# Optimization experiments

Measured on AMD Instinct MI355X. Metric: run time of the kernel, lower is better.

The kernel has to match this reference:

```python
import jax, jax.numpy as jnp
import numpy as np

TOP_K = 2


def setup_inputs() -> dict:
    key = jax.random.key(0)
    ks = jax.random.split(key, 5)
    T, H, I, E = 4096, 2048, 4096, 8
    scale = 0.02
    return {
        "hidden_states": jax.random.normal(ks[0], (T, H), dtype=jnp.float32),
        "router_logits": jax.random.normal(ks[1], (T, E), dtype=jnp.float32),
        "w1": jax.random.normal(ks[2], (E, I, H), dtype=jnp.float32) * scale,
        "w3": jax.random.normal(ks[3], (E, I, H), dtype=jnp.float32) * scale,
        "w2": jax.random.normal(ks[4], (E, H, I), dtype=jnp.float32) * scale,
    }


def reference(hidden_states, router_logits, w1, w3, w2):
    # hidden_states: [T, H], router_logits: [T, E]
    E = w1.shape[0]
    # Top-k routing with softmax renormalization over the selected logits.
    topk_vals, topk_idx = jax.lax.top_k(router_logits, TOP_K)  # [T, K]
    routing_weights = jax.nn.softmax(topk_vals, axis=-1)       # [T, K]
    # combine[t, e] = sum of routing weights of slots that picked expert e
    combine = jnp.sum(
        jnp.where(topk_idx[:, :, None] == jnp.arange(E)[None, None, :],
                  routing_weights[:, :, None], 0.0),
        axis=1)  # [T, E]
    out = jnp.zeros_like(hidden_states)
    for e in range(E):  # fixed small structural loop over experts
        gate = hidden_states @ w1[e].T        # [T, I]
        up = hidden_states @ w3[e].T          # [T, I]
        y = (jax.nn.silu(gate) * up) @ w2[e].T  # [T, H]
        out = out + combine[:, e, None] * y
    return out
```

## Files before the change

### kernel.cpp

```cpp
#include <hip/hip_runtime.h>
#include <stdint.h>

#define T_TOK 4096
#define H_DIM 2048
#define I_DIM 4096
#define N_EXP 8

typedef __attribute__((ext_vector_type(8))) short bf16x8;
typedef __attribute__((ext_vector_type(4))) float f32x4;
typedef __attribute__((ext_vector_type(8))) unsigned short u16x8;

__device__ __forceinline__ unsigned short f2bf(float x) {
    union { float f; unsigned u; } v; v.f = x;
    unsigned r = v.u + 0x7FFF + ((v.u >> 16) & 1);
    return (unsigned short)(r >> 16);
}

__device__ __forceinline__ u16x8 cvt8(float4 a, float4 b) {
    u16x8 o;
    o[0] = f2bf(a.x); o[1] = f2bf(a.y); o[2] = f2bf(a.z); o[3] = f2bf(a.w);
    o[4] = f2bf(b.x); o[5] = f2bf(b.y); o[6] = f2bf(b.z); o[7] = f2bf(b.w);
    return o;
}

__device__ __forceinline__ void async_cp16(const void* g, const unsigned short* lds_base) {
    __builtin_amdgcn_global_load_lds(
        (const __attribute__((address_space(1))) unsigned*)g,
        (__attribute__((address_space(3))) unsigned*)(unsigned)(uintptr_t)lds_base,
        16, 0, 0);
}

__global__ void routing_kernel(const float* __restrict__ logits,
                               int* __restrict__ counts, int* __restrict__ offsets,
                               int* __restrict__ btok, float* __restrict__ bw,
                               int* __restrict__ tok2slot) {
    __shared__ int s_cnt[N_EXP];
    __shared__ int s_off[N_EXP];
    __shared__ int s_cur[N_EXP];
    const int tid = threadIdx.x;
    if (tid < N_EXP) s_cnt[tid] = 0;
    __syncthreads();

    int e0a[16], e1a[16]; float w0a[16], w1a[16];
    #pragma unroll
    for (int it = 0; it < 16; ++it) {
        int t = tid + it * 256;
        float l[8];
        #pragma unroll
        for (int e = 0; e < 8; ++e) l[e] = logits[t * 8 + e];
        int b0 = 0; float v0 = l[0];
        #pragma unroll
        for (int e = 1; e < 8; ++e) if (l[e] > v0) { v0 = l[e]; b0 = e; }
        int b1 = (b0 == 0) ? 1 : 0; float v1 = l[b1];
        #pragma unroll
        for (int e = 0; e < 8; ++e) if (e != b0 && l[e] > v1) { v1 = l[e]; b1 = e; }
        float w0 = 1.0f / (1.0f + __expf(v1 - v0));
        e0a[it] = b0; e1a[it] = b1; w0a[it] = w0; w1a[it] = 1.0f - w0;
        atomicAdd(&s_cnt[b0], 1);
        atomicAdd(&s_cnt[b1], 1);
    }
    __syncthreads();
    if (tid == 0) {
        int acc = 0;
        for (int e = 0; e < N_EXP; ++e) { s_off[e] = acc; s_cur[e] = acc; acc += s_cnt[e]; }
    }
    __syncthreads();
    if (tid < N_EXP) { counts[tid] = s_cnt[tid]; offsets[tid] = s_off[tid]; }
    #pragma unroll
    for (int it = 0; it < 16; ++it) {
        int t = tid + it * 256;
        int p0 = atomicAdd(&s_cur[e0a[it]], 1);
        btok[p0] = t; bw[p0] = w0a[it];
        int p1 = atomicAdd(&s_cur[e1a[it]], 1);
        btok[p1] = t; bw[p1] = w1a[it];
        tok2slot[2 * t] = p0;
        tok2slot[2 * t + 1] = p1;
    }
}

__global__ void cvt_kernel(const float* __restrict__ x, unsigned short* __restrict__ xb) {
    int i = blockIdx.x * blockDim.x + threadIdx.x;
    float4 a = ((const float4*)x)[2 * i];
    float4 b = ((const float4*)x)[2 * i + 1];
    ((u16x8*)xb)[i] = cvt8(a, b);
}


__global__ __launch_bounds__(256, 2)
void gemm1p_kernel(const unsigned short* __restrict__ Xb,
                   const float* __restrict__ W1,
                   const float* __restrict__ W3,
                   const int* __restrict__ counts,
                   const int* __restrict__ offsets,
                   const int* __restrict__ btok,
                   unsigned short* __restrict__ hbuf) {
    const int e = blockIdx.z;
    const int ne = counts[e];
    const int mt = blockIdx.y;
    if (mt * 128 >= ne) return;
    const int nt = blockIdx.x;
    const int off = offsets[e];

    __shared__ unsigned short sA[3][128 * 32];
    __shared__ unsigned short sB1[3][128 * 32];
    __shared__ unsigned short sB3[3][128 * 32];

    const int tid = threadIdx.x;
    const int lane = tid & 63;
    const int wv = tid >> 6;
    const int wm = (wv >> 1) << 6;
    const int wn = (wv & 1) << 6;
    const int q = lane >> 4;
    const int c = lane & 15;
    const int xq = q ^ ((c >> 1) & 3);

    const int aoff = (wm + c) * 32 + xq * 8;
    const int boff = (wn + c) * 32 + xq * 8;

    const int arow = wv * 16 + (lane >> 2);
    const int sgA = (lane & 3) ^ ((lane >> 3) & 3);

    int sl0 = mt * 128 + arow;       if (sl0 >= ne) sl0 = ne - 1;
    int sl1 = mt * 128 + arow + 64;  if (sl1 >= ne) sl1 = ne - 1;
    const unsigned short* gA0 = Xb + (size_t)btok[off + sl0] * H_DIM + sgA * 8;
    const unsigned short* gA1 = Xb + (size_t)btok[off + sl1] * H_DIM + sgA * 8;
    const int dofsA0 = wv * 512;
    const int dofsA1 = 2048 + wv * 512;

    const int brow = tid >> 2;
    const int sgB = (tid & 3) ^ ((tid >> 3) & 3);
    const size_t wrow = (size_t)e * I_DIM + nt * 128 + brow;
    const float* gW1  = W1 + wrow * H_DIM + (tid & 3) * 8;
    const float* gW1b = gW1 + (size_t)64 * H_DIM;
    const float* gW3  = W3 + wrow * H_DIM + (tid & 3) * 8;
    const float* gW3b = gW3 + (size_t)64 * H_DIM;
    const int bwro  = brow * 32 + sgB * 8;
    const int bwro2 = bwro + 2048;

    f32x4 accg[4][4], accu[4][4];
    const f32x4 zero = {0.0f, 0.0f, 0.0f, 0.0f};
    #pragma unroll
    for (int i = 0; i < 4; ++i)
        #pragma unroll
        for (int j = 0; j < 4; ++j) { accg[i][j] = zero; accu[i][j] = zero; }

    float4 w0, w1, w2, w3, w4, w5, w6, w7;

    #pragma unroll
    for (int h = 0; h < 2; ++h) {
        const float* p1  = gW1  + h * 32;
        const float* p1b = gW1b + h * 32;
        const float* p3  = gW3  + h * 32;
        const float* p3b = gW3b + h * 32;
        *(u16x8*)(&sB1[h][bwro])  = cvt8(((const float4*)p1)[0],  ((const float4*)p1)[1]);
        *(u16x8*)(&sB1[h][bwro2]) = cvt8(((const float4*)p1b)[0], ((const float4*)p1b)[1]);
        *(u16x8*)(&sB3[h][bwro])  = cvt8(((const float4*)p3)[0],  ((const float4*)p3)[1]);
        *(u16x8*)(&sB3[h][bwro2]) = cvt8(((const float4*)p3b)[0], ((const float4*)p3b)[1]);
    }
    async_cp16(gA0,      &sA[0][dofsA0]);
    async_cp16(gA1,      &sA[0][dofsA1]);
    async_cp16(gA0 + 32, &sA[1][dofsA0]);
    async_cp16(gA1 + 32, &sA[1][dofsA1]);
    w0 = ((const float4*)(gW1  + 64))[0]; w1 = ((const float4*)(gW1  + 64))[1];
    w2 = ((const float4*)(gW1b + 64))[0]; w3 = ((const float4*)(gW1b + 64))[1];
    w4 = ((const float4*)(gW3  + 64))[0]; w5 = ((const float4*)(gW3  + 64))[1];
    w6 = ((const float4*)(gW3b + 64))[0]; w7 = ((const float4*)(gW3b + 64))[1];

    asm volatile("s_waitcnt lgkmcnt(0)" ::: "memory");
    asm volatile("s_waitcnt vmcnt(10)" ::: "memory");
    __builtin_amdgcn_s_barrier();
    __builtin_amdgcn_sched_barrier(0);

    const int NT = H_DIM / 32;

#define G1_PH(H, S, S2)                                                                              \
    {                                                                                                \
        if ((H) + 2 < NT) {                                                                          \
            *(u16x8*)(&sB1[S2][bwro])  = cvt8(w0, w1);                                               \
            *(u16x8*)(&sB1[S2][bwro2]) = cvt8(w2, w3);                                               \
            *(u16x8*)(&sB3[S2][bwro])  = cvt8(w4, w5);                                               \
            *(u16x8*)(&sB3[S2][bwro2]) = cvt8(w6, w7);                                               \
        }                                                                                            \
        if ((H) + 3 < NT) {                                                                          \
            const float* p1  = gW1  + (size_t)((H) + 3) * 32;                                        \
            const float* p1b = gW1b + (size_t)((H) + 3) * 32;                                        \
            const float* p3  = gW3  + (size_t)((H) + 3) * 32;                                        \
            const float* p3b = gW3b + (size_t)((H) + 3) * 32;                                        \
            w0 = ((const float4*)p1)[0];  w1 = ((const float4*)p1)[1];                               \
            w2 = ((const float4*)p1b)[0]; w3 = ((const float4*)p1b)[1];                              \
            w4 = ((const float4*)p3)[0];  w5 = ((const float4*)p3)[1];                               \
            w6 = ((const float4*)p3b)[0]; w7 = ((const float4*)p3b)[1];                              \
        }                                                                                            \
        bf16x8 af[4], b1f[4], b3f[4];                                                                \
        _Pragma("unroll")                                                                            \
        for (int i = 0; i < 4; ++i) af[i]  = *(const bf16x8*)(&sA[S][aoff + i * 512]);               \
        _Pragma("unroll")                                                                            \
        for (int j = 0; j < 4; ++j) b1f[j] = *(const bf16x8*)(&sB1[S][boff + j * 512]);              \
        _Pragma("unroll")                                                                            \
        for (int j = 0; j < 4; ++j) b3f[j] = *(const bf16x8*)(&sB3[S][boff + j * 512]);              \
        if ((H) + 2 < NT) {                                                                          \
            async_cp16(gA0 + ((H) + 2) * 32, &sA[S2][dofsA0]);                                       \
            async_cp16(gA1 + ((H) + 2) * 32, &sA[S2][dofsA1]);                                       \
        }                                                                                            \
        __builtin_amdgcn_sched_barrier(0);                                                           \
        __builtin_amdgcn_s_setprio(1);                                                               \
        _Pragma("unroll")                                                                            \
        for (int i = 0; i < 4; ++i)                                                                  \
            _Pragma("unroll")                                                                        \
            for (int j = 0; j < 4; ++j)                                                              \
                accg[i][j] = __builtin_amdgcn_mfma_f32_16x16x32_bf16(af[i], b1f[j], accg[i][j], 0, 0, 0); \
        _Pragma("unroll")                                                                            \
        for (int i = 0; i < 4; ++i)                                                                  \
            _Pragma("unroll")                                                                        \
            for (int j = 0; j < 4; ++j)                                                              \
                accu[i][j] = __builtin_amdgcn_mfma_f32_16x16x32_bf16(af[i], b3f[j], accu[i][j], 0, 0, 0); \
        __builtin_amdgcn_s_setprio(0);                                                               \
        if ((H) + 1 < NT) {                                                                          \
            asm volatile("s_waitcnt lgkmcnt(0)" ::: "memory");                                       \
            if ((H) + 3 < NT)      asm volatile("s_waitcnt vmcnt(10)" ::: "memory");                 \
            else if ((H) + 2 < NT) asm volatile("s_waitcnt vmcnt(2)" ::: "memory");                  \
            else                   asm volatile("s_waitcnt vmcnt(0)" ::: "memory");                  \
            __builtin_amdgcn_s_barrier();                                                            \
            __builtin_amdgcn_sched_barrier(0);                                                       \
        }                                                                                            \
    }

    int h = 0;
    for (int t = 0; t < 21; ++t) {
        G1_PH(h,     0, 2);
        G1_PH(h + 1, 1, 0);
        G1_PH(h + 2, 2, 1);
        h += 3;
    }
    G1_PH(63, 0, 2);
#undef G1_PH

    #pragma unroll
    for (int i = 0; i < 4; ++i) {
        #pragma unroll
        for (int r = 0; r < 4; ++r) {
            int mloc = wm + i * 16 + q * 4 + r;
            int slot = mt * 128 + mloc;
            if (slot < ne) {
                size_t rowbase = (size_t)(off + slot) * I_DIM + nt * 128 + wn;
                #pragma unroll
                for (int j = 0; j < 4; ++j) {
                    float g = accg[i][j][r];
                    float u = accu[i][j][r];
                    float val = (g / (1.0f + __expf(-g))) * u;
                    hbuf[rowbase + j * 16 + c] = f2bf(val);
                }
            }
        }
    }
}

__global__ __launch_bounds__(256, 3)
void gemm2p_kernel(const unsigned short* __restrict__ hbuf,
                   const float* __restrict__ W2,
                   const int* __restrict__ counts,
                   const int* __restrict__ offsets,
                   const int* __restrict__ btok,
                   const float* __restrict__ bw,
                   float* __restrict__ out) {
    const int e = blockIdx.z;
    const int ne = counts[e];
    const int mt = blockIdx.y;
    if (mt * 128 >= ne) return;
    const int nt = blockIdx.x;
    const int off = offsets[e];

    __shared__ unsigned short sA[3][128 * 32];
    __shared__ unsigned short sB[3][128 * 32];

    const int tid = threadIdx.x;
    const int lane = tid & 63;
    const int wv = tid >> 6;
    const int wm = (wv >> 1) << 6;
    const int wn = (wv & 1) << 6;
    const int q = lane >> 4;
    const int c = lane & 15;
    const int xq = q ^ ((c >> 1) & 3);

    const int aoff = (wm + c) * 32 + xq * 8;
    const int boff = (wn + c) * 32 + xq * 8;

    const int arow = wv * 16 + (lane >> 2);
    const int sgA = (lane & 3) ^ ((lane >> 3) & 3);
    int sl0 = mt * 128 + arow;       if (sl0 >= ne) sl0 = ne - 1;
    int sl1 = mt * 128 + arow + 64;  if (sl1 >= ne) sl1 = ne - 1;
    const unsigned short* gA0 = hbuf + (size_t)(off + sl0) * I_DIM + sgA * 8;
    const unsigned short* gA1 = hbuf + (size_t)(off + sl1) * I_DIM + sgA * 8;
    const int dofsA0 = wv * 512;
    const int dofsA1 = 2048 + wv * 512;

    const int brow = tid >> 2;
    const int sgB = (tid & 3) ^ ((tid >> 3) & 3);
    const size_t wrow = (size_t)e * H_DIM + nt * 128 + brow;
    const float* gB  = W2 + wrow * I_DIM + (tid & 3) * 8;
    const float* gBb = gB + (size_t)64 * I_DIM;
    const int bwro  = brow * 32 + sgB * 8;
    const int bwro2 = bwro + 2048;

    f32x4 acc[4][4];
    const f32x4 zero = {0.0f, 0.0f, 0.0f, 0.0f};
    #pragma unroll
    for (int i = 0; i < 4; ++i)
        #pragma unroll
        for (int j = 0; j < 4; ++j) acc[i][j] = zero;

    float4 w0, w1, w2, w3;

    #pragma unroll
    for (int h = 0; h < 2; ++h) {
        const float* p  = gB  + h * 32;
        const float* pb = gBb + h * 32;
        *(u16x8*)(&sB[h][bwro])  = cvt8(((const float4*)p)[0],  ((const float4*)p)[1]);
        *(u16x8*)(&sB[h][bwro2]) = cvt8(((const float4*)pb)[0], ((const float4*)pb)[1]);
    }
    async_cp16(gA0,      &sA[0][dofsA0]);
    async_cp16(gA1,      &sA[0][dofsA1]);
    async_cp16(gA0 + 32, &sA[1][dofsA0]);
    async_cp16(gA1 + 32, &sA[1][dofsA1]);
    w0 = ((const float4*)(gB  + 64))[0]; w1 = ((const float4*)(gB  + 64))[1];
    w2 = ((const float4*)(gBb + 64))[0]; w3 = ((const float4*)(gBb + 64))[1];

    asm volatile("s_waitcnt lgkmcnt(0)" ::: "memory");
    asm volatile("s_waitcnt vmcnt(6)" ::: "memory");
    __builtin_amdgcn_s_barrier();
    __builtin_amdgcn_sched_barrier(0);

    const int NT = I_DIM / 32;

#define G2_PH(H, S, S2)                                                                              \
    {                                                                                                \
        if ((H) + 2 < NT) {                                                                          \
            *(u16x8*)(&sB[S2][bwro])  = cvt8(w0, w1);                                                \
            *(u16x8*)(&sB[S2][bwro2]) = cvt8(w2, w3);                                                \
        }                                                                                            \
        if ((H) + 3 < NT) {                                                                          \
            const float* p  = gB  + (size_t)((H) + 3) * 32;                                          \
            const float* pb = gBb + (size_t)((H) + 3) * 32;                                          \
            w0 = ((const float4*)p)[0];  w1 = ((const float4*)p)[1];                                 \
            w2 = ((const float4*)pb)[0]; w3 = ((const float4*)pb)[1];                                \
        }                                                                                            \
        bf16x8 af[4], bfr[4];                                                                        \
        _Pragma("unroll")                                                                            \
        for (int i = 0; i < 4; ++i) af[i]  = *(const bf16x8*)(&sA[S][aoff + i * 512]);               \
        _Pragma("unroll")                                                                            \
        for (int j = 0; j < 4; ++j) bfr[j] = *(const bf16x8*)(&sB[S][boff + j * 512]);               \
        if ((H) + 2 < NT) {                                                                          \
            async_cp16(gA0 + ((H) + 2) * 32, &sA[S2][dofsA0]);                                       \
            async_cp16(gA1 + ((H) + 2) * 32, &sA[S2][dofsA1]);                                       \
        }                                                                                            \
        __builtin_amdgcn_sched_barrier(0);                                                           \
        __builtin_amdgcn_s_setprio(1);                                                               \
        _Pragma("unroll")                                                                            \
        for (int i = 0; i < 4; ++i)                                                                  \
            _Pragma("unroll")                                                                        \
            for (int j = 0; j < 4; ++j)                                                              \
                acc[i][j] = __builtin_amdgcn_mfma_f32_16x16x32_bf16(af[i], bfr[j], acc[i][j], 0, 0, 0); \
        __builtin_amdgcn_s_setprio(0);                                                               \
        if ((H) + 1 < NT) {                                                                          \
            asm volatile("s_waitcnt lgkmcnt(0)" ::: "memory");                                       \
            if ((H) + 3 < NT)      asm volatile("s_waitcnt vmcnt(6)" ::: "memory");                  \
            else if ((H) + 2 < NT) asm volatile("s_waitcnt vmcnt(2)" ::: "memory");                  \
            else                   asm volatile("s_waitcnt vmcnt(0)" ::: "memory");                  \
            __builtin_amdgcn_s_barrier();                                                            \
            __builtin_amdgcn_sched_barrier(0);                                                       \
        }                                                                                            \
    }

    int h = 0;
    for (int t = 0; t < 42; ++t) {
        G2_PH(h,     0, 2);
        G2_PH(h + 1, 1, 0);
        G2_PH(h + 2, 2, 1);
        h += 3;
    }
    G2_PH(126, 0, 2);
    G2_PH(127, 1, 0);
#undef G2_PH

    #pragma unroll
    for (int i = 0; i < 4; ++i) {
        #pragma unroll
        for (int r = 0; r < 4; ++r) {
            int mloc = wm + i * 16 + q * 4 + r;
            int slot = mt * 128 + mloc;
            if (slot < ne) {
                int tok = btok[off + slot];
                float wgt = bw[off + slot];
                float* obase = out + (size_t)tok * H_DIM + nt * 128 + wn;
                #pragma unroll
                for (int j = 0; j < 4; ++j)
                    atomicAdd(obase + j * 16 + c, wgt * acc[i][j][r]);
            }
        }
    }
}


__global__ __launch_bounds__(256, 2)
void gemm1_kernel(const unsigned short* __restrict__ Xb,
                  const float* __restrict__ W1,
                  const float* __restrict__ W3,
                  const int* __restrict__ counts,
                  const int* __restrict__ offsets,
                  const int* __restrict__ btok,
                  unsigned short* __restrict__ hbuf) {
    const int e = blockIdx.z;
    const int ne = counts[e];
    const int mt = blockIdx.y;
    if (mt * 128 >= ne) return;
    const int nt = blockIdx.x;
    const int off = offsets[e];

    __shared__ unsigned short sA[128][32];
    __shared__ unsigned short sB1[128][32];
    __shared__ unsigned short sB3[128][32];
    __shared__ int s_tok[128];

    const int tid = threadIdx.x;
    if (tid < 128) {
        int slot = mt * 128 + tid;
        s_tok[tid] = (slot < ne) ? btok[off + slot] : -1;
    }

    const float* __restrict__ pB1 = W1 + (size_t)e * I_DIM * H_DIM + (size_t)(nt * 128) * H_DIM;
    const float* __restrict__ pB3 = W3 + (size_t)e * I_DIM * H_DIM + (size_t)(nt * 128) * H_DIM;

    const int lane = tid & 63;
    const int wv = tid >> 6;
    const int wm = (wv >> 1) << 6;
    const int wn = (wv & 1) << 6;
    const int q = lane >> 4;
    const int c = lane & 15;

    f32x4 accg[4][4], accu[4][4];
    const f32x4 zero = {0.0f, 0.0f, 0.0f, 0.0f};
    #pragma unroll
    for (int i = 0; i < 4; ++i)
        #pragma unroll
        for (int j = 0; j < 4; ++j) { accg[i][j] = zero; accu[i][j] = zero; }

    const int srow = tid >> 2;
    const int schunk = (tid & 3) * 8;

    for (int kt = 0; kt < H_DIM; kt += 32) {
        __syncthreads();
        #pragma unroll
        for (int p = 0; p < 2; ++p) {
            int r = srow + p * 64;
            int tok = s_tok[r];
            u16x8 av = {0, 0, 0, 0, 0, 0, 0, 0};
            if (tok >= 0)
                av = *(const u16x8*)(Xb + (size_t)tok * H_DIM + kt + schunk);
            *(u16x8*)(&sA[r][schunk]) = av;

            const float* b1 = pB1 + (size_t)r * H_DIM + kt + schunk;
            *(u16x8*)(&sB1[r][schunk]) = cvt8(*(const float4*)(b1), *(const float4*)(b1 + 4));

            const float* b3 = pB3 + (size_t)r * H_DIM + kt + schunk;
            *(u16x8*)(&sB3[r][schunk]) = cvt8(*(const float4*)(b3), *(const float4*)(b3 + 4));
        }
        __syncthreads();

        bf16x8 af[4], b1f[4], b3f[4];
        #pragma unroll
        for (int i = 0; i < 4; ++i)
            af[i] = *(const bf16x8*)(&sA[wm + i * 16 + c][q * 8]);
        #pragma unroll
        for (int j = 0; j < 4; ++j) {
            b1f[j] = *(const bf16x8*)(&sB1[wn + j * 16 + c][q * 8]);
            b3f[j] = *(const bf16x8*)(&sB3[wn + j * 16 + c][q * 8]);
        }
        #pragma unroll
        for (int i = 0; i < 4; ++i)
            #pragma unroll
            for (int j = 0; j < 4; ++j) {
                accg[i][j] = __builtin_amdgcn_mfma_f32_16x16x32_bf16(af[i], b1f[j], accg[i][j], 0, 0, 0);
                accu[i][j] = __builtin_amdgcn_mfma_f32_16x16x32_bf16(af[i], b3f[j], accu[i][j], 0, 0, 0);
            }
    }

    #pragma unroll
    for (int i = 0; i < 4; ++i) {
        #pragma unroll
        for (int r = 0; r < 4; ++r) {
            int mloc = wm + i * 16 + q * 4 + r;
            int slot = mt * 128 + mloc;
            if (slot < ne) {
                size_t rowbase = (size_t)(off + slot) * I_DIM + nt * 128 + wn;
                #pragma unroll
                for (int j = 0; j < 4; ++j) {
                    float g = accg[i][j][r];
                    float u = accu[i][j][r];
                    float val = (g / (1.0f + __expf(-g))) * u;
                    hbuf[rowbase + j * 16 + c] = f2bf(val);
                }
            }
        }
    }
}

__global__ __launch_bounds__(256, 2)
void gemm2_kernel(const unsigned short* __restrict__ hbuf,
                  const float* __restrict__ W2,
                  const int* __restrict__ counts,
                  const int* __restrict__ offsets,
                  const int* __restrict__ btok,
                  const float* __restrict__ bw,
                  float* __restrict__ out) {
    const int e = blockIdx.z;
    const int ne = counts[e];
    const int mt = blockIdx.y;
    if (mt * 128 >= ne) return;
    const int nt = blockIdx.x;
    const int off = offsets[e];

    __shared__ unsigned short sA[128][32];
    __shared__ unsigned short sB[128][32];

    const int tid = threadIdx.x;
    const int lane = tid & 63;
    const int wv = tid >> 6;
    const int wm = (wv >> 1) << 6;
    const int wn = (wv & 1) << 6;
    const int q = lane >> 4;
    const int c = lane & 15;

    const float* __restrict__ pB = W2 + (size_t)e * H_DIM * I_DIM + (size_t)(nt * 128) * I_DIM;

    f32x4 acc[4][4];
    const f32x4 zero = {0.0f, 0.0f, 0.0f, 0.0f};
    #pragma unroll
    for (int i = 0; i < 4; ++i)
        #pragma unroll
        for (int j = 0; j < 4; ++j) acc[i][j] = zero;

    const int srow = tid >> 2;
    const int schunk = (tid & 3) * 8;

    for (int kt = 0; kt < I_DIM; kt += 32) {
        __syncthreads();
        #pragma unroll
        for (int p = 0; p < 2; ++p) {
            int r = srow + p * 64;
            int slot = mt * 128 + r;
            u16x8 av = {0, 0, 0, 0, 0, 0, 0, 0};
            if (slot < ne)
                av = *(const u16x8*)(hbuf + (size_t)(off + slot) * I_DIM + kt + schunk);
            *(u16x8*)(&sA[r][schunk]) = av;

            const float* b = pB + (size_t)r * I_DIM + kt + schunk;
            *(u16x8*)(&sB[r][schunk]) = cvt8(*(const float4*)(b), *(const float4*)(b + 4));
        }
        __syncthreads();

        bf16x8 af[4], bfr[4];
        #pragma unroll
        for (int i = 0; i < 4; ++i)
            af[i] = *(const bf16x8*)(&sA[wm + i * 16 + c][q * 8]);
        #pragma unroll
        for (int j = 0; j < 4; ++j)
            bfr[j] = *(const bf16x8*)(&sB[wn + j * 16 + c][q * 8]);
        #pragma unroll
        for (int i = 0; i < 4; ++i)
            #pragma unroll
            for (int j = 0; j < 4; ++j)
                acc[i][j] = __builtin_amdgcn_mfma_f32_16x16x32_bf16(af[i], bfr[j], acc[i][j], 0, 0, 0);
    }

    #pragma unroll
    for (int i = 0; i < 4; ++i) {
        #pragma unroll
        for (int r = 0; r < 4; ++r) {
            int mloc = wm + i * 16 + q * 4 + r;
            int slot = mt * 128 + mloc;
            if (slot < ne) {
                int tok = btok[off + slot];
                float wgt = bw[off + slot];
                float* obase = out + (size_t)tok * H_DIM + nt * 128 + wn;
                #pragma unroll
                for (int j = 0; j < 4; ++j)
                    atomicAdd(obase + j * 16 + c, wgt * acc[i][j][r]);
            }
        }
    }
}


extern "C" void kernel_launch(void* const* d_in, const int* in_sizes, int n_in,
                              void* d_out, int out_size, void* d_ws, size_t ws_size,
                              hipStream_t stream) {
    const float* hs = (const float*)d_in[0];
    const float* rl = (const float*)d_in[1];
    const float* w1 = (const float*)d_in[2];
    const float* w3 = (const float*)d_in[3];
    const float* w2 = (const float*)d_in[4];
    float* out = (float*)d_out;

    char* ws = (char*)d_ws;
    int*   counts   = (int*)(ws);
    int*   offsets  = (int*)(ws + 256);
    int*   btok     = (int*)(ws + 4096);
    float* bw       = (float*)(ws + 36864);
    int*   tok2slot = (int*)(ws + 69632);

    const size_t MB = 1ull << 20;
    const size_t NEED_A = 146 * MB;

    if (ws_size >= NEED_A) {
        unsigned short* Xb   = (unsigned short*)(ws + 1 * MB);
        unsigned short* hbuf = (unsigned short*)(ws + 17 * MB);

        hipMemsetAsync(out, 0, (size_t)T_TOK * H_DIM * sizeof(float), stream);

        routing_kernel<<<1, 256, 0, stream>>>(rl, counts, offsets, btok, bw, tok2slot);

        cvt_kernel<<<(T_TOK * H_DIM / 8) / 256, 256, 0, stream>>>(hs, Xb);

        gemm1p_kernel<<<dim3(I_DIM / 128, 64, N_EXP), 256, 0, stream>>>(
            Xb, w1, w3, counts, offsets, btok, hbuf);

        gemm2p_kernel<<<dim3(H_DIM / 128, 64, N_EXP), 256, 0, stream>>>(
            hbuf, w2, counts, offsets, btok, bw, out);
    } else {
        unsigned short* Xb   = (unsigned short*)(ws + 1 * MB);
        unsigned short* hbuf = (unsigned short*)(ws + 32 * MB);

        hipMemsetAsync(out, 0, (size_t)T_TOK * H_DIM * sizeof(float), stream);

        routing_kernel<<<1, 256, 0, stream>>>(rl, counts, offsets, btok, bw, tok2slot);

        cvt_kernel<<<(T_TOK * H_DIM / 8) / 256, 256, 0, stream>>>(hs, Xb);

        gemm1_kernel<<<dim3(I_DIM / 128, T_TOK / 128, N_EXP), 256, 0, stream>>>(
            Xb, w1, w3, counts, offsets, btok, hbuf);

        gemm2_kernel<<<dim3(H_DIM / 128, T_TOK / 128, N_EXP), 256, 0, stream>>>(
            hbuf, w2, counts, offsets, btok, bw, out);
    }
}
```

Measured before the change: 1.245 ms.

## Widen gemm2p output tile to 256 columns for more A-tile reuse

Doubles the N tile of the down-projection GEMM from 128 to 256 columns. Each warp now computes a 64x128 sub-tile with twice as many MFMA accumulators, and each block loads and converts four W2 row groups per K step. The aim is to reuse each loaded hbuf A tile across twice as many output columns, halving A traffic and the block count. In exchange it raises register and LDS use (occupancy bound drops from 3 to 2) and halves the number of blocks in the grid.

```diff
diff --git a/kernel.cpp b/kernel.cpp
--- a/kernel.cpp
+++ b/kernel.cpp
@@ -255,7 +255,7 @@
     }
 }
 
-__global__ __launch_bounds__(256, 3)
+__global__ __launch_bounds__(256, 2)
 void gemm2p_kernel(const unsigned short* __restrict__ hbuf,
                    const float* __restrict__ W2,
                    const int* __restrict__ counts,
@@ -271,13 +271,13 @@
     const int off = offsets[e];
 
     __shared__ unsigned short sA[3][128 * 32];
-    __shared__ unsigned short sB[3][128 * 32];
+    __shared__ unsigned short sB[3][256 * 32];
 
     const int tid = threadIdx.x;
     const int lane = tid & 63;
     const int wv = tid >> 6;
     const int wm = (wv >> 1) << 6;
-    const int wn = (wv & 1) << 6;
+    const int wn = (wv & 1) << 7;
     const int q = lane >> 4;
     const int c = lane & 15;
     const int xq = q ^ ((c >> 1) & 3);
@@ -296,37 +296,44 @@
 
     const int brow = tid >> 2;
     const int sgB = (tid & 3) ^ ((tid >> 3) & 3);
-    const size_t wrow = (size_t)e * H_DIM + nt * 128 + brow;
-    const float* gB  = W2 + wrow * I_DIM + (tid & 3) * 8;
-    const float* gBb = gB + (size_t)64 * I_DIM;
+    const size_t wrow = (size_t)e * H_DIM + nt * 256 + brow;
+    const float* gB0 = W2 + wrow * I_DIM + (tid & 3) * 8;
+    const float* gB1 = gB0 + (size_t)64  * I_DIM;
+    const float* gB2 = gB0 + (size_t)128 * I_DIM;
+    const float* gB3 = gB0 + (size_t)192 * I_DIM;
     const int bwro  = brow * 32 + sgB * 8;
-    const int bwro2 = bwro + 2048;
-
-    f32x4 acc[4][4];
+
+    f32x4 acc[4][8];
     const f32x4 zero = {0.0f, 0.0f, 0.0f, 0.0f};
     #pragma unroll
     for (int i = 0; i < 4; ++i)
         #pragma unroll
-        for (int j = 0; j < 4; ++j) acc[i][j] = zero;
-
-    float4 w0, w1, w2, w3;
+        for (int j = 0; j < 8; ++j) acc[i][j] = zero;
+
+    float4 w0, w1, w2, w3, w4, w5, w6, w7;
 
     #pragma unroll
     for (int h = 0; h < 2; ++h) {
-        const float* p  = gB  + h * 32;
-        const float* pb = gBb + h * 32;
-        *(u16x8*)(&sB[h][bwro])  = cvt8(((const float4*)p)[0],  ((const float4*)p)[1]);
-        *(u16x8*)(&sB[h][bwro2]) = cvt8(((const float4*)pb)[0], ((const float4*)pb)[1]);
+        const float* p0 = gB0 + h * 32;
+        const float* p1 = gB1 + h * 32;
+        const float* p2 = gB2 + h * 32;
+        const float* p3 = gB3 + h * 32;
+        *(u16x8*)(&sB[h][bwro])        = cvt8(((const float4*)p0)[0], ((const float4*)p0)[1]);
+        *(u16x8*)(&sB[h][bwro + 2048]) = cvt8(((const float4*)p1)[0], ((const float4*)p1)[1]);
+        *(u16x8*)(&sB[h][bwro + 4096]) = cvt8(((const float4*)p2)[0], ((const float4*)p2)[1]);
+        *(u16x8*)(&sB[h][bwro + 6144]) = cvt8(((const float4*)p3)[0], ((const float4*)p3)[1]);
     }
     async_cp16(gA0,      &sA[0][dofsA0]);
     async_cp16(gA1,      &sA[0][dofsA1]);
     async_cp16(gA0 + 32, &sA[1][dofsA0]);
     async_cp16(gA1 + 32, &sA[1][dofsA1]);
-    w0 = ((const float4*)(gB  + 64))[0]; w1 = ((const float4*)(gB  + 64))[1];
-    w2 = ((const float4*)(gBb + 64))[0]; w3 = ((const float4*)(gBb + 64))[1];
+    w0 = ((const float4*)(gB0 + 64))[0]; w1 = ((const float4*)(gB0 + 64))[1];
+    w2 = ((const float4*)(gB1 + 64))[0]; w3 = ((const float4*)(gB1 + 64))[1];
+    w4 = ((const float4*)(gB2 + 64))[0]; w5 = ((const float4*)(gB2 + 64))[1];
+    w6 = ((const float4*)(gB3 + 64))[0]; w7 = ((const float4*)(gB3 + 64))[1];
 
     asm volatile("s_waitcnt lgkmcnt(0)" ::: "memory");
-    asm volatile("s_waitcnt vmcnt(6)" ::: "memory");
+    asm volatile("s_waitcnt vmcnt(10)" ::: "memory");
     __builtin_amdgcn_s_barrier();
     __builtin_amdgcn_sched_barrier(0);
 
@@ -335,20 +342,26 @@
 #define G2_PH(H, S, S2)                                                                              \
     {                                                                                                \
         if ((H) + 2 < NT) {                                                                          \
-            *(u16x8*)(&sB[S2][bwro])  = cvt8(w0, w1);                                                \
-            *(u16x8*)(&sB[S2][bwro2]) = cvt8(w2, w3);                                                \
+            *(u16x8*)(&sB[S2][bwro])        = cvt8(w0, w1);                                          \
+            *(u16x8*)(&sB[S2][bwro + 2048]) = cvt8(w2, w3);                                          \
+            *(u16x8*)(&sB[S2][bwro + 4096]) = cvt8(w4, w5);                                          \
+            *(u16x8*)(&sB[S2][bwro + 6144]) = cvt8(w6, w7);                                          \
         }                                                                                            \
         if ((H) + 3 < NT) {                                                                          \
-            const float* p  = gB  + (size_t)((H) + 3) * 32;                                          \
-            const float* pb = gBb + (size_t)((H) + 3) * 32;                                          \
-            w0 = ((const float4*)p)[0];  w1 = ((const float4*)p)[1];                                 \
-            w2 = ((const float4*)pb)[0]; w3 = ((const float4*)pb)[1];                                \
-        }                                                                                            \
-        bf16x8 af[4], bfr[4];                                                                        \
+            const float* p0 = gB0 + (size_t)((H) + 3) * 32;                                          \
+            const float* p1 = gB1 + (size_t)((H) + 3) * 32;                                          \
+            const float* p2 = gB2 + (size_t)((H) + 3) * 32;                                          \
+            const float* p3 = gB3 + (size_t)((H) + 3) * 32;                                          \
+            w0 = ((const float4*)p0)[0]; w1 = ((const float4*)p0)[1];                                \
+            w2 = ((const float4*)p1)[0]; w3 = ((const float4*)p1)[1];                                \
+            w4 = ((const float4*)p2)[0]; w5 = ((const float4*)p2)[1];                                \
+            w6 = ((const float4*)p3)[0]; w7 = ((const float4*)p3)[1];                                \
+        }                                                                                            \
+        bf16x8 af[4], bfr[8];                                                                        \
         _Pragma("unroll")                                                                            \
         for (int i = 0; i < 4; ++i) af[i]  = *(const bf16x8*)(&sA[S][aoff + i * 512]);               \
         _Pragma("unroll")                                                                            \
-        for (int j = 0; j < 4; ++j) bfr[j] = *(const bf16x8*)(&sB[S][boff + j * 512]);               \
+        for (int j = 0; j < 8; ++j) bfr[j] = *(const bf16x8*)(&sB[S][boff + j * 512]);               \
         if ((H) + 2 < NT) {                                                                          \
             async_cp16(gA0 + ((H) + 2) * 32, &sA[S2][dofsA0]);                                       \
             async_cp16(gA1 + ((H) + 2) * 32, &sA[S2][dofsA1]);                                       \
@@ -358,12 +371,12 @@
         _Pragma("unroll")                                                                            \
         for (int i = 0; i < 4; ++i)                                                                  \
             _Pragma("unroll")                                                                        \
-            for (int j = 0; j < 4; ++j)                                                              \
+            for (int j = 0; j < 8; ++j)                                                              \
                 acc[i][j] = __builtin_amdgcn_mfma_f32_16x16x32_bf16(af[i], bfr[j], acc[i][j], 0, 0, 0); \
         __builtin_amdgcn_s_setprio(0);                                                               \
         if ((H) + 1 < NT) {                                                                          \
             asm volatile("s_waitcnt lgkmcnt(0)" ::: "memory");                                       \
-            if ((H) + 3 < NT)      asm volatile("s_waitcnt vmcnt(6)" ::: "memory");                  \
+            if ((H) + 3 < NT)      asm volatile("s_waitcnt vmcnt(10)" ::: "memory");                 \
             else if ((H) + 2 < NT) asm volatile("s_waitcnt vmcnt(2)" ::: "memory");                  \
             else                   asm volatile("s_waitcnt vmcnt(0)" ::: "memory");                  \
             __builtin_amdgcn_s_barrier();                                                            \
@@ -391,9 +404,9 @@
             if (slot < ne) {
                 int tok = btok[off + slot];
                 float wgt = bw[off + slot];
-                float* obase = out + (size_t)tok * H_DIM + nt * 128 + wn;
+                float* obase = out + (size_t)tok * H_DIM + nt * 256 + wn;
                 #pragma unroll
-                for (int j = 0; j < 4; ++j)
+                for (int j = 0; j < 8; ++j)
                     atomicAdd(obase + j * 16 + c, wgt * acc[i][j][r]);
             }
         }
@@ -624,7 +637,7 @@
         gemm1p_kernel<<<dim3(I_DIM / 128, 64, N_EXP), 256, 0, stream>>>(
             Xb, w1, w3, counts, offsets, btok, hbuf);
 
-        gemm2p_kernel<<<dim3(H_DIM / 128, 64, N_EXP), 256, 0, stream>>>(
+        gemm2p_kernel<<<dim3(H_DIM / 256, 64, N_EXP), 256, 0, stream>>>(
             hbuf, w2, counts, offsets, btok, bw, out);
     } else {
         unsigned short* Xb   = (unsigned short*)(ws + 1 * MB);
```

Result: slower. 1.334 ms (+7.2%).
